# Kernel optimization log

Measured on AMD Instinct MI355X. Metric: run time of the kernel, lower is better.

## Reference

```python
import jax, jax.numpy as jnp
import numpy as np
from jax import lax


def ste_round(x):
    # straight-through rounding (matches brevitas STE)
    return x + lax.stop_gradient(jnp.round(x) - x)


def fq_signed(x, bits=8):
    """Per-tensor symmetric signed fake-quant (weights / QuantIdentity input)."""
    qmax = 2.0 ** (bits - 1) - 1.0
    scale = lax.stop_gradient(jnp.max(jnp.abs(x)) / qmax + 1e-12)
    q = jnp.clip(ste_round(x / scale), -qmax - 1.0, qmax)
    return q * scale, scale


def fq_unsigned(x, bits=8):
    """Per-tensor unsigned fake-quant used by QuantReLU (input already >= 0)."""
    qmax = 2.0 ** bits - 1.0
    scale = lax.stop_gradient(jnp.max(x) / qmax + 1e-12)
    q = jnp.clip(ste_round(x / scale), 0.0, qmax)
    return q * scale, scale


def fq_bias_int32(b, in_scale, w_scale):
    # Int32Bias: bias quantized at scale = input_scale * weight_scale
    s = in_scale * w_scale
    q = jnp.clip(ste_round(b / s), -2.0 ** 31, 2.0 ** 31 - 1.0)
    return q * s


def conv2d(x, w):
    # x: NCHW, w: OIHW, stride 1, VALID padding
    return lax.conv_general_dilated(x, w, (1, 1), 'VALID',
                                    dimension_numbers=('NCHW', 'OIHW', 'NCHW'))


def max_pool2(x):
    return lax.reduce_window(x, -jnp.inf, lax.max, (1, 1, 2, 2), (1, 1, 2, 2), 'VALID')


def setup_inputs() -> dict:
    key = jax.random.key(0)
    ks = jax.random.split(key, 9)
    B = 8192
    x = jax.random.normal(ks[0], (B, 3, 32, 32), dtype=jnp.float32)
    w1 = jax.random.normal(ks[1], (6, 3, 5, 5), dtype=jnp.float32) * 0.1
    b1 = jax.random.normal(ks[2], (6,), dtype=jnp.float32) * 0.05
    w2 = jax.random.normal(ks[3], (16, 6, 5, 5), dtype=jnp.float32) * 0.08
    b2 = jax.random.normal(ks[4], (16,), dtype=jnp.float32) * 0.05
    fw1 = jax.random.normal(ks[5], (120, 400), dtype=jnp.float32) * 0.05
    fb1 = jax.random.normal(ks[6], (120,), dtype=jnp.float32) * 0.05
    fw2 = jax.random.normal(ks[7], (10, 120), dtype=jnp.float32) * 0.09
    fb2 = jax.random.normal(ks[8], (10,), dtype=jnp.float32) * 0.05
    return {"x": x, "w1": w1, "b1": b1, "w2": w2, "b2": b2,
            "fw1": fw1, "fb1": fb1, "fw2": fw2, "fb2": fb2}


def reference(x, w1, b1, w2, b2, fw1, fb1, fw2, fb2):
    # QuantIdentity: signed 8-bit fake-quant of the input
    xq, a_scale = fq_signed(x, 8)

    # conv1 + QuantReLU + maxpool
    w1q, w1s = fq_signed(w1, 8)
    b1q = fq_bias_int32(b1, a_scale, w1s)
    out = conv2d(xq, w1q) + b1q[None, :, None, None]          # [B,6,28,28]
    out, a_scale = fq_unsigned(jax.nn.relu(out), 8)
    out = max_pool2(out)                                       # [B,6,14,14]

    # conv2 + QuantReLU + maxpool
    w2q, w2s = fq_signed(w2, 8)
    b2q = fq_bias_int32(b2, a_scale, w2s)
    out = conv2d(out, w2q) + b2q[None, :, None, None]          # [B,16,10,10]
    out, a_scale = fq_unsigned(jax.nn.relu(out), 8)
    out = max_pool2(out)                                       # [B,16,5,5]

    out = out.reshape(out.shape[0], -1)                        # [B,400]

    # fc1 + QuantReLU
    fw1q, fw1s = fq_signed(fw1, 8)
    fb1q = fq_bias_int32(fb1, a_scale, fw1s)
    out = out @ fw1q.T + fb1q                                  # [B,120]
    out, a_scale = fq_unsigned(jax.nn.relu(out), 8)

    # fc2
    fw2q, fw2s = fq_signed(fw2, 8)
    fb2q = fq_bias_int32(fb2, a_scale, fw2s)
    out = out @ fw2q.T + fb2q                                  # [B,10]
    return out
```

## Files before the change

### kernel.cpp

```cpp
#include <hip/hip_runtime.h>
#include <stdint.h>

#define DI __device__ __forceinline__

static constexpr size_t OFF_MAX  = 0;
static constexpr size_t OFF_WSC  = 64;
static constexpr size_t OFF_W1P  = 1024;
static constexpr size_t OFF_W2P  = 4096;
static constexpr size_t OFF_WS2  = 8192;
static constexpr size_t OFF_FW1B = 8704;
static constexpr size_t OFF_FW2I = 212992;
static constexpr size_t OFF_XBM  = 221184;
static constexpr size_t OFF_UF   = 262144;
static constexpr size_t OFF_T2F  = OFF_UF + 4194304ull;
static constexpr size_t OFF_T1F  = OFF_UF + 20971520ull;

#if defined(__HIP_DEVICE_COMPILE__) && __has_builtin(__builtin_amdgcn_sdot4)
#define HAS_SDOT4 1
#else
#define HAS_SDOT4 0
#endif

DI int dot4(int a, int b, int c) {
#if HAS_SDOT4
  return __builtin_amdgcn_sdot4(a, b, c, false);
#else
  c += ((int)(a << 24) >> 24) * ((int)(b << 24) >> 24);
  c += ((int)(a << 16) >> 24) * ((int)(b << 16) >> 24);
  c += ((int)(a << 8) >> 24) * ((int)(b << 8) >> 24);
  c += ((int)a >> 24) * ((int)b >> 24);
  return c;
#endif
}

DI float warpMax(float v) {
#pragma unroll
  for (int o = 32; o > 0; o >>= 1) v = fmaxf(v, __shfl_down(v, o, 64));
  return v;
}

DI float blockMax(float v) {
  __shared__ float sm[8];
  int lane = threadIdx.x & 63, w = threadIdx.x >> 6;
  v = warpMax(v);
  if (lane == 0) sm[w] = v;
  __syncthreads();
  if (w == 0) {
    int nw = blockDim.x >> 6;
    v = (lane < nw) ? sm[lane] : 0.0f;
    v = warpMax(v);
  }
  return v;
}

DI int qclamp(float v, float s) {
  return (int)fminf(fmaxf(rintf(v / s), -128.0f), 127.0f);
}

DI uint32_t pack3(float a, float b, float c, float s) {
  int qa = qclamp(a, s), qb = qclamp(b, s), qc = qclamp(c, s);
  return (uint32_t)(qa & 255) | ((uint32_t)(qb & 255) << 8) | ((uint32_t)(qc & 255) << 16);
}

__global__ __launch_bounds__(256) void k_prep(const float4* __restrict__ x,
                                              const float* __restrict__ w1, const float* __restrict__ w2,
                                              const float* __restrict__ fw1, const float* __restrict__ fw2,
                                              int* __restrict__ mx, float* __restrict__ wsc,
                                              int* __restrict__ w1pi, int* __restrict__ w2pi,
                                              float* __restrict__ fw2i, int* __restrict__ wsum2,
                                              float* __restrict__ fw1bm, float* __restrict__ xbmax) {
  int tid = threadIdx.x;
  int bid = blockIdx.x;
  if (bid < 1024) {
    const int n4 = 6291456;
    float m = 0.f;
    for (int i = bid * 256 + tid; i < n4; i += 1024 * 256) {
      float4 v = x[i];
      m = fmaxf(m, fmaxf(fmaxf(fabsf(v.x), fabsf(v.y)), fmaxf(fabsf(v.z), fabsf(v.w))));
    }
    m = blockMax(m);
    if (tid == 0) xbmax[bid] = m;
    return;
  }
  if (bid < 1040) {
    int sl = bid - 1024;
    const float4* f4 = (const float4*)fw1;
    float m = 0.f;
    for (int i = sl * 750 + tid; i < (sl + 1) * 750; i += 256) {
      float4 v = f4[i];
      m = fmaxf(m, fmaxf(fmaxf(fabsf(v.x), fabsf(v.y)), fmaxf(fabsf(v.z), fabsf(v.w))));
    }
    m = blockMax(m);
    if (tid == 0) fw1bm[sl] = m;
    return;
  }

  __shared__ float sbc;
  __shared__ int wsm[16];
  int wbid = bid - 1040;

  if (wbid == 0) {
    if (tid < 4) mx[tid] = 0;
    float m = 0.f;
    for (int i = tid; i < 450; i += 256) m = fmaxf(m, fabsf(w1[i]));
    m = blockMax(m);
    if (tid == 0) { sbc = m; wsc[0] = m / 127.0f + 1e-12f; }
    __syncthreads();
    float s = sbc / 127.0f + 1e-12f;
    if (tid < 150) {
      int o = tid / 25, t = tid % 25;
      int q0 = qclamp(w1[o * 75 + 0 * 25 + t], s);
      int q1 = qclamp(w1[o * 75 + 1 * 25 + t], s);
      int q2 = qclamp(w1[o * 75 + 2 * 25 + t], s);
      w1pi[tid] = (q0 & 255) | ((q1 & 255) << 8) | ((q2 & 255) << 16);
    }
  } else if (wbid == 1) {
    float m = 0.0f;
    for (int i = tid; i < 2400; i += 256) m = fmaxf(m, fabsf(w2[i]));
    m = blockMax(m);
    if (tid == 0) { sbc = m; wsc[1] = m / 127.0f + 1e-12f; }
    if (tid < 16) wsm[tid] = 0;
    __syncthreads();
    float s = sbc / 127.0f + 1e-12f;
    for (int t0 = tid; t0 < 400; t0 += 256) {
      int o = t0 / 25, t = t0 % 25;
      int q0 = qclamp(w2[o * 150 + 0 * 25 + t], s);
      int q1 = qclamp(w2[o * 150 + 1 * 25 + t], s);
      int q2 = qclamp(w2[o * 150 + 2 * 25 + t], s);
      int q3 = qclamp(w2[o * 150 + 3 * 25 + t], s);
      int q4 = qclamp(w2[o * 150 + 4 * 25 + t], s);
      int q5 = qclamp(w2[o * 150 + 5 * 25 + t], s);
      w2pi[2 * t0] = (q0 & 255) | ((q1 & 255) << 8) | ((q2 & 255) << 16) | ((q3 & 255) << 24);
      w2pi[2 * t0 + 1] = (q4 & 255) | ((q5 & 255) << 8);
      atomicAdd(&wsm[o], q0 + q1 + q2 + q3 + q4 + q5);
    }
    __syncthreads();
    if (tid < 16) wsum2[tid] = wsm[tid];
  } else {
    float m = 0.0f;
    for (int i = tid; i < 1200; i += 256) m = fmaxf(m, fabsf(fw2[i]));
    m = blockMax(m);
    if (tid == 0) { sbc = m; wsc[3] = m / 127.0f + 1e-12f; }
    __syncthreads();
    float s = sbc / 127.0f + 1e-12f;
    for (int i = tid; i < 1200; i += 256)
      fw2i[i] = fminf(fmaxf(rintf(fw2[i] / s), -128.0f), 127.0f);
  }
}

__global__ __launch_bounds__(256, 6) void k_conv1x(const float4* __restrict__ x4, const int* __restrict__ w1pi,
                                                   const float* __restrict__ b1, const float* __restrict__ xbmax,
                                                   const float* __restrict__ wsc, float* __restrict__ t1f,
                                                   int* __restrict__ mx1) {
  __shared__ int xl[4608];
  __shared__ float s0sh;
  int tid = threadIdx.x;
  int blk = blockIdx.x;

  float mxv = 0.f;
#pragma unroll
  for (int i = 0; i < 4; ++i) mxv = fmaxf(mxv, xbmax[i * 256 + tid]);
  mxv = blockMax(mxv);
  if (tid == 0) s0sh = mxv / 127.0f + 1e-12f;
  __syncthreads();
  float s0 = s0sh;

  const float4* xb = x4 + (size_t)blk * 3072;
#pragma unroll
  for (int i = 0; i < 4; ++i) {
    int G = i * 256 + tid;
    int img = G >> 8, p4 = G & 255;
    float4 va = xb[img * 768 + p4];
    float4 vb = xb[img * 768 + 256 + p4];
    float4 vc = xb[img * 768 + 512 + p4];
    int4 o;
    o.x = (int)pack3(va.x, vb.x, vc.x, s0);
    o.y = (int)pack3(va.y, vb.y, vc.y, s0);
    o.z = (int)pack3(va.z, vb.z, vc.z, s0);
    o.w = (int)pack3(va.w, vb.w, vc.w, s0);
    int row = p4 >> 3, cg = p4 & 7;
    *(int4*)&xl[img * 1152 + row * 36 + cg * 4] = o;
  }
  __syncthreads();

  float s = s0 * wsc[0];
  float bq[6];
#pragma unroll
  for (int o = 0; o < 6; ++o) bq[o] = rintf(b1[o] / s) * s;

  float lmax = 0.f;
  for (int it = 0; it < 4; ++it) {
    int u = it * 256 + tid;
    if (u < 784) {
      int img = u / 196, rem = u % 196;
      int ph = rem / 14, pw = rem % 14;
      const int* xbase = &xl[img * 1152 + ph * 72 + pw * 2];
      int p[6][6];
#pragma unroll
      for (int r = 0; r < 6; ++r) {
        int2 a0 = *(const int2*)(xbase + r * 36);
        int2 a1 = *(const int2*)(xbase + r * 36 + 2);
        int2 a2 = *(const int2*)(xbase + r * 36 + 4);
        p[r][0] = a0.x; p[r][1] = a0.y; p[r][2] = a1.x;
        p[r][3] = a1.y; p[r][4] = a2.x; p[r][5] = a2.y;
      }
      int bg = blk * 4 + img;
#pragma unroll
      for (int o = 0; o < 6; ++o) {
        const int* wp = w1pi + o * 25;
        int aA0 = 0, aA1 = 0, aB0 = 0, aB1 = 0;
#pragma unroll
        for (int r = 0; r < 6; ++r) {
#pragma unroll
          for (int tc = 0; tc < 5; ++tc) {
            if (r <= 4) {
              int w = wp[r * 5 + tc];
              aA0 = dot4(p[r][tc], w, aA0);
              aA1 = dot4(p[r][tc + 1], w, aA1);
            }
            if (r >= 1) {
              int w = wp[(r - 1) * 5 + tc];
              aB0 = dot4(p[r][tc], w, aB0);
              aB1 = dot4(p[r][tc + 1], w, aB1);
            }
          }
        }
        int m0 = max(max(aA0, aA1), max(aB0, aB1));
        float v0 = fmaxf((float)m0 * s + bq[o], 0.f);
        t1f[(size_t)(o * 8192 + bg) * 196 + ph * 14 + pw] = v0;
        lmax = fmaxf(lmax, v0);
      }
    }
  }
  lmax = blockMax(lmax);
  if (tid == 0) atomicMax(mx1, __float_as_int(lmax));
}

__global__ __launch_bounds__(256, 4) void k_conv2q(const float* __restrict__ t1f, const int* __restrict__ w2pi,
                                                   const float* __restrict__ b2, const float* __restrict__ mxf,
                                                   const float* __restrict__ wsc, const int* __restrict__ wsum2,
                                                   float* __restrict__ t2fb, int* __restrict__ mx2) {
  __shared__ char t1l[25344];
  __shared__ int w2l[800];
  __shared__ int ws2l[16];
  int tid = threadIdx.x, blk = blockIdx.x;
  for (int i = tid; i < 800; i += 256) w2l[i] = w2pi[i];
  if (tid < 16) ws2l[tid] = wsum2[tid];

  float s1 = mxf[1] / 255.0f + 1e-12f;
  int b0 = blk * 16;
  const float4* tf = (const float4*)t1f;
  for (int it = 0; it < 19; ++it) {
    int g = it * 256 + tid;
    if (g < 4704) {
      int oc = g / 784, rem = g % 784;
      int img = rem / 49, f4 = rem % 49;
      float4 v = tf[(size_t)(oc * 8192 + b0 + img) * 49 + f4];
      int pos = f4 * 4;
      float vv[4] = {v.x, v.y, v.z, v.w};
#pragma unroll
      for (int c = 0; c < 4; ++c) {
        int pp = pos + c;
        int row = pp / 14, px = pp - row * 14;
        int q = (int)fminf(fmaxf(rintf(vv[c] / s1), 0.f), 255.f) - 128;
        t1l[img * 1584 + row * 112 + px * 8 + oc] = (char)q;
      }
    }
  }
  __syncthreads();

  float s = s1 * wsc[1];
  float lmax = 0.f;
  for (int it = 0; it < 3; ++it) {
    int u = it * 256 + tid;
    if (u < 640) {
      int pair = u & 7;
      int t = u >> 3;
      int ph = t % 5, img = t / 5;
      const char* base = &t1l[img * 1584 + ph * 224];
      int aA[2][10], aB[2][10];
#pragma unroll
      for (int g = 0; g < 2; ++g)
#pragma unroll
        for (int j = 0; j < 10; ++j) { aA[g][j] = 0; aB[g][j] = 0; }

#pragma unroll 1
      for (int r = 0; r < 6; ++r) {
        int p2[28];
        const uint4* rp = (const uint4*)(base + r * 112);
#pragma unroll
        for (int q = 0; q < 7; ++q) {
          uint4 uu = rp[q];
          p2[4 * q] = (int)uu.x; p2[4 * q + 1] = (int)uu.y;
          p2[4 * q + 2] = (int)uu.z; p2[4 * q + 3] = (int)uu.w;
        }
        if (r <= 4) {
#pragma unroll
          for (int tc = 0; tc < 5; ++tc) {
#pragma unroll
            for (int g = 0; g < 2; ++g) {
              int2 w = *(const int2*)&w2l[(pair * 2 + g) * 50 + r * 10 + 2 * tc];
#pragma unroll
              for (int j = 0; j < 10; ++j)
                aA[g][j] = dot4(p2[2 * (j + tc) + 1], w.y, dot4(p2[2 * (j + tc)], w.x, aA[g][j]));
            }
          }
        }
        if (r >= 1) {
#pragma unroll
          for (int tc = 0; tc < 5; ++tc) {
#pragma unroll
            for (int g = 0; g < 2; ++g) {
              int2 w = *(const int2*)&w2l[(pair * 2 + g) * 50 + (r - 1) * 10 + 2 * tc];
#pragma unroll
              for (int j = 0; j < 10; ++j)
                aB[g][j] = dot4(p2[2 * (j + tc) + 1], w.y, dot4(p2[2 * (j + tc)], w.x, aB[g][j]));
            }
          }
        }
      }
      int bg = b0 + img;
#pragma unroll
      for (int g = 0; g < 2; ++g) {
        int oc = pair * 2 + g;
        int off = 128 * ws2l[oc];
        float bq = rintf(b2[oc] / s) * s;
        float* orow = t2fb + (size_t)bg * 400 + oc * 25 + ph * 5;
#pragma unroll
        for (int j = 0; j < 5; ++j) {
          int m4 = max(max(aA[g][2 * j], aA[g][2 * j + 1]), max(aB[g][2 * j], aB[g][2 * j + 1]));
          float v = fmaxf((float)(m4 + off) * s + bq, 0.f);
          orow[j] = v;
          lmax = fmaxf(lmax, v);
        }
      }
    }
  }
  lmax = blockMax(lmax);
  if (tid == 0) atomicMax(mx2, __float_as_int(lmax));
}

__global__ __launch_bounds__(256) void k_fc1q(const float* __restrict__ t2fb, const float* __restrict__ fw1,
                                              const float* __restrict__ fb1, const float* __restrict__ mxf,
                                              const float* __restrict__ fw1bm, float* __restrict__ u,
                                              int* __restrict__ mx3) {
  __shared__ int wl[12000];
  __shared__ int xq[3200];
  __shared__ int wsl[120];
  __shared__ float fwssh;
  int tid = threadIdx.x, blk = blockIdx.x;

  if (tid < 64) {
    float m = (tid < 16) ? fw1bm[tid] : 0.f;
    m = warpMax(m);
    if (tid == 0) fwssh = m / 127.0f + 1e-12f;
  }
  __syncthreads();
  float fws = fwssh;

  const float4* w4 = (const float4*)fw1;
  for (int i = tid; i < 12000; i += 256) {
    float4 v = w4[i];
    int q0 = qclamp(v.x, fws), q1 = qclamp(v.y, fws), q2 = qclamp(v.z, fws), q3 = qclamp(v.w, fws);
    wl[i] = (q0 & 255) | ((q1 & 255) << 8) | ((q2 & 255) << 16) | ((q3 & 255) << 24);
  }

  float s2 = mxf[2] / 255.0f + 1e-12f;
  int b0 = blk * 32;
  const float4* tf = (const float4*)t2fb + (size_t)b0 * 100;
  for (int it = 0; it < 13; ++it) {
    int g = it * 256 + tid;
    if (g < 3200) {
      float4 v = tf[g];
      int q0 = (int)fminf(fmaxf(rintf(v.x / s2), 0.f), 255.f) - 128;
      int q1 = (int)fminf(fmaxf(rintf(v.y / s2), 0.f), 255.f) - 128;
      int q2 = (int)fminf(fmaxf(rintf(v.z / s2), 0.f), 255.f) - 128;
      int q3 = (int)fminf(fmaxf(rintf(v.w / s2), 0.f), 255.f) - 128;
      xq[g] = (q0 & 255) | ((q1 & 255) << 8) | ((q2 & 255) << 16) | ((q3 & 255) << 24);
    }
  }
  __syncthreads();

  if (tid < 120) {
    int acc = 0;
    const int* row = &wl[tid * 100];
#pragma unroll
    for (int c = 0; c < 100; c += 4) {
      int4 wv = *(const int4*)&row[c];
      acc = dot4(wv.x, 0x01010101, acc);
      acc = dot4(wv.y, 0x01010101, acc);
      acc = dot4(wv.z, 0x01010101, acc);
      acc = dot4(wv.w, 0x01010101, acc);
    }
    wsl[tid] = acc;
  }
  __syncthreads();

  float s = s2 * fws;
  int img8 = tid >> 3, j = tid & 7;
  int acc[15];
#pragma unroll
  for (int seg = 0; seg < 15; ++seg) acc[seg] = 0;
#pragma unroll 1
  for (int kc = 0; kc < 5; ++kc) {
    int xr[20];
#pragma unroll
    for (int q = 0; q < 5; ++q) {
      int4 t = *(const int4*)&xq[img8 * 100 + kc * 20 + q * 4];
      xr[4 * q] = t.x; xr[4 * q + 1] = t.y; xr[4 * q + 2] = t.z; xr[4 * q + 3] = t.w;
    }
#pragma unroll
    for (int seg = 0; seg < 15; ++seg) {
      const int* wrow = &wl[(seg * 8 + j) * 100 + kc * 20];
#pragma unroll
      for (int q = 0; q < 20; q += 4) {
        int4 wv = *(const int4*)&wrow[q];
        acc[seg] = dot4(xr[q], wv.x, acc[seg]);
        acc[seg] = dot4(xr[q + 1], wv.y, acc[seg]);
        acc[seg] = dot4(xr[q + 2], wv.z, acc[seg]);
        acc[seg] = dot4(xr[q + 3], wv.w, acc[seg]);
      }
    }
  }
  float lmax = 0.f;
  int bg = b0 + img8;
#pragma unroll
  for (int seg = 0; seg < 15; ++seg) {
    int oc = seg * 8 + j;
    int tot = acc[seg] + 128 * wsl[oc];
    float bq = rintf(fb1[oc] / s) * s;
    float v = fmaxf((float)tot * s + bq, 0.f);
    u[(size_t)bg * 120 + oc] = v;
    lmax = fmaxf(lmax, v);
  }
  lmax = blockMax(lmax);
  if (tid == 0) atomicMax(mx3, __float_as_int(lmax));
}

__global__ __launch_bounds__(64) void k_fc2(const float* __restrict__ u, const float* __restrict__ fw2i,
                                            const float* __restrict__ fb2, const float* __restrict__ mxf,
                                            const float* __restrict__ wsc, float* __restrict__ out) {
  int b = blockIdx.x * 64 + threadIdx.x;
  float s3 = mxf[3] / 255.0f + 1e-12f;
  float s = s3 * wsc[3];
  float acc[10];
#pragma unroll
  for (int o = 0; o < 10; ++o) acc[o] = 0.f;
  const float4* ur = (const float4*)(u + (size_t)b * 120);
  for (int kk = 0; kk < 30; ++kk) {
    float4 v = ur[kk];
    float q0 = fminf(fmaxf(rintf(v.x / s3), 0.f), 255.f);
    float q1 = fminf(fmaxf(rintf(v.y / s3), 0.f), 255.f);
    float q2 = fminf(fmaxf(rintf(v.z / s3), 0.f), 255.f);
    float q3 = fminf(fmaxf(rintf(v.w / s3), 0.f), 255.f);
#pragma unroll
    for (int o = 0; o < 10; ++o) {
      const float4* wr = (const float4*)(fw2i + o * 120 + kk * 4);
      float4 wv = wr[0];
      acc[o] = fmaf(q0, wv.x, acc[o]);
      acc[o] = fmaf(q1, wv.y, acc[o]);
      acc[o] = fmaf(q2, wv.z, acc[o]);
      acc[o] = fmaf(q3, wv.w, acc[o]);
    }
  }
#pragma unroll
  for (int o = 0; o < 10; ++o) {
    float bq = rintf(fb2[o] / s) * s;
    out[(size_t)b * 10 + o] = acc[o] * s + bq;
  }
}

extern "C" void kernel_launch(void* const* d_in, const int* in_sizes, int n_in,
                              void* d_out, int out_size, void* d_ws, size_t ws_size,
                              hipStream_t stream) {
  const float* x = (const float*)d_in[0];
  const float* w1 = (const float*)d_in[1];
  const float* b1 = (const float*)d_in[2];
  const float* w2 = (const float*)d_in[3];
  const float* b2 = (const float*)d_in[4];
  const float* fw1 = (const float*)d_in[5];
  const float* fb1 = (const float*)d_in[6];
  const float* fw2 = (const float*)d_in[7];
  const float* fb2 = (const float*)d_in[8];

  char* ws = (char*)d_ws;
  int* mx = (int*)(ws + OFF_MAX);
  float* mxf = (float*)(ws + OFF_MAX);
  float* wsc = (float*)(ws + OFF_WSC);
  int* w1pi = (int*)(ws + OFF_W1P);
  int* w2pi = (int*)(ws + OFF_W2P);
  int* wsum2 = (int*)(ws + OFF_WS2);
  float* fw1bm = (float*)(ws + OFF_FW1B);
  float* fw2i = (float*)(ws + OFF_FW2I);
  float* xbmax = (float*)(ws + OFF_XBM);
  float* uf = (float*)(ws + OFF_UF);
  float* t2fb = (float*)(ws + OFF_T2F);
  float* t1f = (float*)(ws + OFF_T1F);
  float* out = (float*)d_out;

  k_prep<<<1043, 256, 0, stream>>>((const float4*)x, w1, w2, fw1, fw2, mx, wsc,
                                   w1pi, w2pi, fw2i, wsum2, fw1bm, xbmax);
  k_conv1x<<<2048, 256, 0, stream>>>((const float4*)x, w1pi, b1, xbmax, wsc, t1f, mx + 1);
  k_conv2q<<<512, 256, 0, stream>>>(t1f, w2pi, b2, mxf, wsc, wsum2, t2fb, mx + 2);
  k_fc1q<<<256, 256, 0, stream>>>(t2fb, fw1, fb1, mxf, fw1bm, uf, mx + 3);
  k_fc2<<<128, 64, 0, stream>>>(uf, fw2i, fb2, mxf, wsc, out);
}
```

Before: 158.2 us.

## Compute conv1 with int8 MFMA instead of per-thread sdot4 loops

Rewrites the conv1 kernel so each wavefront handles one image and computes the 5x5x3 convolution as an im2col matrix product on the int8 MFMA 16x16x64 instruction. Rows are the 4 pool positions times 4 window offsets and columns are output channels padded from 6 to 16, with the pooling max taken across the accumulator lanes. This replaces the scalar dot4 chains. In exchange, 10 of the 16 MFMA output columns are wasted padding, the LDS gathers become scattered, and there are 49 serial tiles per wave with small stores.

```diff
diff --git a/kernel.cpp b/kernel.cpp
--- a/kernel.cpp
+++ b/kernel.cpp
@@ -2,6 +2,8 @@
 #include <stdint.h>
 
 #define DI __device__ __forceinline__
+
+typedef __attribute__((ext_vector_type(4))) int i32x4;
 
 static constexpr size_t OFF_MAX  = 0;
 static constexpr size_t OFF_WSC  = 64;
@@ -148,14 +150,15 @@
   }
 }
 
-__global__ __launch_bounds__(256, 6) void k_conv1x(const float4* __restrict__ x4, const int* __restrict__ w1pi,
-                                                   const float* __restrict__ b1, const float* __restrict__ xbmax,
-                                                   const float* __restrict__ wsc, float* __restrict__ t1f,
-                                                   int* __restrict__ mx1) {
+__global__ __launch_bounds__(256) void k_conv1m(const float4* __restrict__ x4, const int* __restrict__ w1pi,
+                                                const float* __restrict__ b1, const float* __restrict__ xbmax,
+                                                const float* __restrict__ wsc, float* __restrict__ t1f,
+                                                int* __restrict__ mx1) {
   __shared__ int xl[4608];
   __shared__ float s0sh;
   int tid = threadIdx.x;
   int blk = blockIdx.x;
+  int lane = tid & 63, wave = tid >> 6;
 
   float mxv = 0.f;
 #pragma unroll
@@ -184,53 +187,73 @@
   __syncthreads();
 
   float s = s0 * wsc[0];
-  float bq[6];
-#pragma unroll
-  for (int o = 0; o < 6; ++o) bq[o] = rintf(b1[o] / s) * s;
-
+
+  int oc = lane & 15;
+  int g = lane >> 4;
+  int r16 = lane & 15;
+  int p_idx = r16 >> 2;
+  int ci = r16 & 3;
+  int drow = ci >> 1, dcol = ci & 1;
+
+  i32x4 wb0, wb1;
+  {
+    int base = oc * 25;
+    int t0 = g * 4;
+    wb0.x = (oc < 6) ? w1pi[base + t0 + 0] : 0;
+    wb0.y = (oc < 6) ? w1pi[base + t0 + 1] : 0;
+    wb0.z = (oc < 6) ? w1pi[base + t0 + 2] : 0;
+    wb0.w = (oc < 6) ? w1pi[base + t0 + 3] : 0;
+    int t1 = 16 + g * 4;
+    wb1.x = (oc < 6 && t1 + 0 < 25) ? w1pi[base + t1 + 0] : 0;
+    wb1.y = (oc < 6 && t1 + 1 < 25) ? w1pi[base + t1 + 1] : 0;
+    wb1.z = (oc < 6 && t1 + 2 < 25) ? w1pi[base + t1 + 2] : 0;
+    wb1.w = (oc < 6 && t1 + 3 < 25) ? w1pi[base + t1 + 3] : 0;
+  }
+
+  int offA0[4], offA1[4];
+  bool pad1[4];
+#pragma unroll
+  for (int j = 0; j < 4; ++j) {
+    int t = g * 4 + j;
+    offA0[j] = (t / 5) * 36 + (t % 5);
+    int t2 = 16 + g * 4 + j;
+    pad1[j] = (t2 > 24);
+    int tt = pad1[j] ? 24 : t2;
+    offA1[j] = (tt / 5) * 36 + (tt % 5);
+  }
+
+  float bqv;
+  {
+    int occ = (oc < 6) ? oc : 5;
+    bqv = rintf(b1[occ] / s) * s;
+  }
+
+  int imgoff = wave * 1152;
+  int bg = blk * 4 + wave;
+  int pr = 0, pc = p_idx;
   float lmax = 0.f;
-  for (int it = 0; it < 4; ++it) {
-    int u = it * 256 + tid;
-    if (u < 784) {
-      int img = u / 196, rem = u % 196;
-      int ph = rem / 14, pw = rem % 14;
-      const int* xbase = &xl[img * 1152 + ph * 72 + pw * 2];
-      int p[6][6];
-#pragma unroll
-      for (int r = 0; r < 6; ++r) {
-        int2 a0 = *(const int2*)(xbase + r * 36);
-        int2 a1 = *(const int2*)(xbase + r * 36 + 2);
-        int2 a2 = *(const int2*)(xbase + r * 36 + 4);
-        p[r][0] = a0.x; p[r][1] = a0.y; p[r][2] = a1.x;
-        p[r][3] = a1.y; p[r][4] = a2.x; p[r][5] = a2.y;
-      }
-      int bg = blk * 4 + img;
-#pragma unroll
-      for (int o = 0; o < 6; ++o) {
-        const int* wp = w1pi + o * 25;
-        int aA0 = 0, aA1 = 0, aB0 = 0, aB1 = 0;
-#pragma unroll
-        for (int r = 0; r < 6; ++r) {
-#pragma unroll
-          for (int tc = 0; tc < 5; ++tc) {
-            if (r <= 4) {
-              int w = wp[r * 5 + tc];
-              aA0 = dot4(p[r][tc], w, aA0);
-              aA1 = dot4(p[r][tc + 1], w, aA1);
-            }
-            if (r >= 1) {
-              int w = wp[(r - 1) * 5 + tc];
-              aB0 = dot4(p[r][tc], w, aB0);
-              aB1 = dot4(p[r][tc + 1], w, aB1);
-            }
-          }
-        }
-        int m0 = max(max(aA0, aA1), max(aB0, aB1));
-        float v0 = fmaxf((float)m0 * s + bq[o], 0.f);
-        t1f[(size_t)(o * 8192 + bg) * 196 + ph * 14 + pw] = v0;
-        lmax = fmaxf(lmax, v0);
-      }
-    }
+
+#pragma unroll 1
+  for (int tile = 0; tile < 49; ++tile) {
+    int base = imgoff + (2 * pr + drow) * 36 + (2 * pc + dcol);
+    i32x4 a0, a1;
+    a0.x = xl[base + offA0[0]];
+    a0.y = xl[base + offA0[1]];
+    a0.z = xl[base + offA0[2]];
+    a0.w = xl[base + offA0[3]];
+    a1.x = pad1[0] ? 0 : xl[base + offA1[0]];
+    a1.y = pad1[1] ? 0 : xl[base + offA1[1]];
+    a1.z = pad1[2] ? 0 : xl[base + offA1[2]];
+    a1.w = pad1[3] ? 0 : xl[base + offA1[3]];
+    i32x4 acc = {0, 0, 0, 0};
+    acc = __builtin_amdgcn_mfma_i32_16x16x64_i8(a0, wb0, acc, 0, 0, 0);
+    acc = __builtin_amdgcn_mfma_i32_16x16x64_i8(a1, wb1, acc, 0, 0, 0);
+    int m = max(max(acc.x, acc.y), max(acc.z, acc.w));
+    float v0 = fmaxf((float)m * s + bqv, 0.f);
+    if (oc < 6) t1f[(size_t)(oc * 8192 + bg) * 196 + tile * 4 + g] = v0;
+    lmax = fmaxf(lmax, (oc < 6) ? v0 : 0.f);
+    pc += 4;
+    if (pc >= 14) { pc -= 14; pr += 1; }
   }
   lmax = blockMax(lmax);
   if (tid == 0) atomicMax(mx1, __float_as_int(lmax));
@@ -500,7 +523,7 @@
 
   k_prep<<<1043, 256, 0, stream>>>((const float4*)x, w1, w2, fw1, fw2, mx, wsc,
                                    w1pi, w2pi, fw2i, wsum2, fw1bm, xbmax);
-  k_conv1x<<<2048, 256, 0, stream>>>((const float4*)x, w1pi, b1, xbmax, wsc, t1f, mx + 1);
+  k_conv1m<<<2048, 256, 0, stream>>>((const float4*)x, w1pi, b1, xbmax, wsc, t1f, mx + 1);
   k_conv2q<<<512, 256, 0, stream>>>(t1f, w2pi, b2, mxf, wsc, wsum2, t2fb, mx + 2);
   k_fc1q<<<256, 256, 0, stream>>>(t2fb, fw1, fb1, mxf, fw1bm, uf, mx + 3);
   k_fc2<<<128, 64, 0, stream>>>(uf, fw2i, fb2, mxf, wsc, out);
```

Measured after the change: 157.6 us. No clear change (-0.4%).
